# Optimization experiments

Hardware: AMD Instinct MI355X
Metric: run time of the kernel (lower is better)

## Reference

```python
import jax, jax.numpy as jnp
import numpy as np

N, E = 10000, 320000
IN_CH, HID, OUT_CH, HEADS = 128, 64, 40, 8
NEG_SLOPE = 0.2


def gat_conv(x, src, dst, W, a_src, a_dst, bias, heads, C, concat, n_nodes):
    # x: [N, F_in]; W: [F_in, heads*C]; a_src/a_dst: [heads, C]
    h = (x @ W).reshape(n_nodes, heads, C)              # [N,H,C]
    alpha_src = jnp.sum(h * a_src, axis=-1)             # [N,H]
    alpha_dst = jnp.sum(h * a_dst, axis=-1)             # [N,H]
    score = jax.nn.leaky_relu(alpha_src[src] + alpha_dst[dst], NEG_SLOPE)  # [E,H]
    # segment softmax over edges sharing the same destination node
    smax = jax.ops.segment_max(score, dst, num_segments=n_nodes)
    smax = jnp.where(jnp.isfinite(smax), smax, 0.0)
    ex = jnp.exp(score - smax[dst])
    denom = jax.ops.segment_sum(ex, dst, num_segments=n_nodes)
    alpha = ex / (denom[dst] + 1e-16)                   # [E,H]
    msg = h[src] * alpha[:, :, None]                    # [E,H,C]
    out = jax.ops.segment_sum(msg, dst, num_segments=n_nodes)  # [N,H,C]
    out = out.reshape(n_nodes, heads * C) if concat else out.mean(axis=1)
    return out + bias


def setup_inputs() -> dict:
    key = jax.random.key(0)
    ks = jax.random.split(key, 16)
    g = 0.1
    return {
        "x": jax.random.normal(ks[0], (N, IN_CH), jnp.float32),
        "edge_index": jax.random.randint(ks[1], (2, E), 0, N, jnp.int64),
        "W1": jax.random.normal(ks[2], (IN_CH, HID), jnp.float32) * g,
        "b1": jnp.zeros((HID,), jnp.float32),
        "Wc1": jax.random.normal(ks[3], (HID, HEADS * HID), jnp.float32) * g,
        "att_src1": jax.random.normal(ks[4], (HEADS, HID), jnp.float32) * g,
        "att_dst1": jax.random.normal(ks[5], (HEADS, HID), jnp.float32) * g,
        "bc1": jnp.zeros((HEADS * HID,), jnp.float32),
        "Wc2": jax.random.normal(ks[6], (HEADS * HID, HID), jnp.float32) * g,
        "att_src2": jax.random.normal(ks[7], (1, HID), jnp.float32) * g,
        "att_dst2": jax.random.normal(ks[8], (1, HID), jnp.float32) * g,
        "bc2": jnp.zeros((HID,), jnp.float32),
        "W2": jax.random.normal(ks[9], (HID, OUT_CH), jnp.float32) * g,
        "b2": jnp.zeros((OUT_CH,), jnp.float32),
    }


def reference(x, edge_index, W1, b1, Wc1, att_src1, att_dst1, bc1,
              Wc2, att_src2, att_dst2, bc2, W2, b2):
    # add self-loops (PyG GATConv default add_self_loops=True)
    loop = jnp.arange(N, dtype=edge_index.dtype)
    src = jnp.concatenate([edge_index[0], loop])
    dst = jnp.concatenate([edge_index[1], loop])

    h = jax.nn.relu(x @ W1 + b1)                                   # lin0 + relu (dropout off in eval)
    h = jax.nn.elu(gat_conv(h, src, dst, Wc1, att_src1, att_dst1, bc1,
                            HEADS, HID, True, N))                  # conv1, concat heads
    h = gat_conv(h, src, dst, Wc2, att_src2, att_dst2, bc2,
                 1, HID, False, N)                                 # conv2, single head
    return h @ W2 + b2
```

## Files before the change

### kernel.cpp

```cpp
#include <hip/hip_runtime.h>
#include <cstdint>
#include <cstddef>

#define IN_CH 128
#define HID 64
#define HEADS 8
#define OUT_CH 40
#define NEG 0.2f
#define PAD 128

typedef __attribute__((ext_vector_type(8))) short bf16x8;
typedef __attribute__((ext_vector_type(4))) float f32x4;

#define MFMA(a, b, c) __builtin_amdgcn_mfma_f32_16x16x32_bf16(a, b, c, 0, 0, 0)

__device__ inline unsigned short f2bf(float f) {
    unsigned u = __float_as_uint(f);
    unsigned r = (u + 0x7FFFu + ((u >> 16) & 1u)) >> 16;
    return (unsigned short)r;
}
__device__ inline float bf2f(unsigned short b) {
    return __uint_as_float((unsigned)b << 16);
}
__device__ inline bf16x8 ldb8(const unsigned short* p) {
    return *reinterpret_cast<const bf16x8*>(p);
}


__global__ void k_init(const float* __restrict__ W1,
                       const float* __restrict__ Wc1, const float* __restrict__ Wc2,
                       const float* __restrict__ as1, const float* __restrict__ ad1,
                       int* __restrict__ cursor,
                       unsigned short* __restrict__ W1T,
                       unsigned short* __restrict__ Wc1T, unsigned short* __restrict__ Wc2T,
                       unsigned short* __restrict__ vaT, int N) {
    int i = blockIdx.x * 256 + threadIdx.x;
    if (i < N) { cursor[i] = 0; return; }
    i -= N;
    if (i < 64 * 128) {
        int j = i >> 7, k = i & 127;
        W1T[i] = f2bf(W1[k * 64 + j]);
        return;
    }
    i -= 64 * 128;
    if (i < 512 * 64) {
        int j = i >> 6, k = i & 63;
        Wc1T[i] = f2bf(Wc1[(size_t)k * 512 + j]);
        return;
    }
    i -= 512 * 64;
    if (i < 64 * 512) {
        int j = i >> 9, k = i & 511;
        Wc2T[i] = f2bf(Wc2[(size_t)k * 64 + j]);
        return;
    }
    i -= 64 * 512;
    if (i < 1024) {
        int t = i >> 6, k = i & 63;
        int h = t & 7;
        const float* a = (t < 8) ? as1 : ad1;
        float sum = 0.f;
        for (int c = 0; c < 64; ++c) sum += Wc1[(size_t)k * 512 + h * 64 + c] * a[h * 64 + c];
        vaT[t * 64 + k] = f2bf(sum);
    }
}


__global__ __launch_bounds__(256) void k_lin1m(const float* __restrict__ x,
                                               const unsigned short* __restrict__ W1T,
                                               const float* __restrict__ b1,
                                               const unsigned short* __restrict__ vaT,
                                               unsigned short* __restrict__ h0b,
                                               float* __restrict__ asrc, float* __restrict__ adst,
                                               const int* __restrict__ ei, int E, int T,
                                               int* __restrict__ cursor, int* __restrict__ csrc,
                                               int N, int NB) {
    __shared__ unsigned short h0s[16][72];
    if (blockIdx.x >= NB) {
        int e = (blockIdx.x - NB) * 256 + threadIdx.x;
        if (e < T) {
            int s, d;
            if (e < E) { s = ei[e]; d = ei[E + e]; } else { s = d = e - E; }
            int pos = atomicAdd(&cursor[d], 1);
            csrc[(size_t)d * PAD + pos] = s;
        }
        return;
    }
    int w = threadIdx.x >> 6, l = threadIdx.x & 63;
    int m0 = blockIdx.x * 16;
    int c = l & 15, g = l >> 4;
    int xr = m0 + c; if (xr >= N) xr = N - 1;
    bf16x8 af[4];
    const float* arow = x + (size_t)xr * 128 + 8 * g;
#pragma unroll
    for (int ks = 0; ks < 4; ++ks) {
        float4 f0 = *(const float4*)(arow + 32 * ks);
        float4 f1 = *(const float4*)(arow + 32 * ks + 4);
        bf16x8 t;
        t[0] = (short)f2bf(f0.x); t[1] = (short)f2bf(f0.y);
        t[2] = (short)f2bf(f0.z); t[3] = (short)f2bf(f0.w);
        t[4] = (short)f2bf(f1.x); t[5] = (short)f2bf(f1.y);
        t[6] = (short)f2bf(f1.z); t[7] = (short)f2bf(f1.w);
        af[ks] = t;
    }
    f32x4 acc = {};
    const unsigned short* brow = W1T + (size_t)(16 * w + c) * 128 + 8 * g;
#pragma unroll
    for (int ks = 0; ks < 4; ++ks) acc = MFMA(af[ks], ldb8(brow + 32 * ks), acc);
    int j = 16 * w + c;
    float bj = b1[j];
#pragma unroll
    for (int r = 0; r < 4; ++r) {
        float v = fmaxf(acc[r] + bj, 0.f);
        unsigned short us = f2bf(v);
        int row = m0 + 4 * g + r;
        if (row < N) h0b[(size_t)row * 64 + j] = us;
        h0s[4 * g + r][j] = us;
    }
    __syncthreads();
    if (w == 0) {
        bf16x8 a0 = ldb8(&h0s[c][8 * g]);
        bf16x8 a1 = ldb8(&h0s[c][32 + 8 * g]);
        bf16x8 b0 = ldb8(&vaT[c * 64 + 8 * g]);
        bf16x8 b1v = ldb8(&vaT[c * 64 + 32 + 8 * g]);
        f32x4 al = {};
        al = MFMA(a0, b0, al);
        al = MFMA(a1, b1v, al);
#pragma unroll
        for (int r = 0; r < 4; ++r) {
            int n = m0 + 4 * g + r;
            if (n < N) {
                if (c < 8) asrc[n * 8 + c] = al[r];
                else       adst[n * 8 + (c - 8)] = al[r];
            }
        }
    }
}


__global__ __launch_bounds__(128) void k_conv1agg(const unsigned short* __restrict__ h0b,
                                                  const float* __restrict__ asrc, const float* __restrict__ adst,
                                                  const int* __restrict__ degs, const int* __restrict__ csrc,
                                                  unsigned short* __restrict__ aggb, int N) {
    __shared__ int srcb[PAD];
    __shared__ float sb[PAD][8];
    __shared__ float mx[8], den[8], adl[8];
    __shared__ float accsh[512];
    int tid = threadIdx.x;
    int n = blockIdx.x;
    int deg = degs[n];
    if (tid < 8) adl[tid] = adst[n * 8 + tid];
    __syncthreads();
    if (tid < deg) {
        int s = csrc[(size_t)n * PAD + tid];
        srcb[tid] = s;
        const float4* ap = (const float4*)&asrc[(size_t)s * 8];
        float4 a0 = ap[0], a1 = ap[1];
        float v;
        v = a0.x + adl[0]; sb[tid][0] = (v >= 0.f) ? v : NEG * v;
        v = a0.y + adl[1]; sb[tid][1] = (v >= 0.f) ? v : NEG * v;
        v = a0.z + adl[2]; sb[tid][2] = (v >= 0.f) ? v : NEG * v;
        v = a0.w + adl[3]; sb[tid][3] = (v >= 0.f) ? v : NEG * v;
        v = a1.x + adl[4]; sb[tid][4] = (v >= 0.f) ? v : NEG * v;
        v = a1.y + adl[5]; sb[tid][5] = (v >= 0.f) ? v : NEG * v;
        v = a1.z + adl[6]; sb[tid][6] = (v >= 0.f) ? v : NEG * v;
        v = a1.w + adl[7]; sb[tid][7] = (v >= 0.f) ? v : NEG * v;
    }
    __syncthreads();
    if (tid < 64) {
        int hh = tid & 7, idx = tid >> 3;
        float m = -1e30f;
        for (int i = idx; i < deg; i += 8) m = fmaxf(m, sb[i][hh]);
        m = fmaxf(m, __shfl_xor(m, 8));
        m = fmaxf(m, __shfl_xor(m, 16));
        m = fmaxf(m, __shfl_xor(m, 32));
        if (tid < 8) mx[tid] = m;
    }
    __syncthreads();
    if (tid < 64) {
        int hh = tid & 7, idx = tid >> 3;
        float mh = mx[hh];
        float d = 0.f;
        for (int i = idx; i < deg; i += 8) {
            float e = __expf(sb[i][hh] - mh);
            sb[i][hh] = e;
            d += e;
        }
        d += __shfl_xor(d, 8);
        d += __shfl_xor(d, 16);
        d += __shfl_xor(d, 32);
        if (tid < 8) den[tid] = d + 1e-16f;
    }
    __syncthreads();
    int lane = tid & 63, wv = tid >> 6;
    int half = lane >> 5, cl = lane & 31;
    float accA[8] = {0.f, 0.f, 0.f, 0.f, 0.f, 0.f, 0.f, 0.f};
    float accB[8] = {0.f, 0.f, 0.f, 0.f, 0.f, 0.f, 0.f, 0.f};
    for (int i = 2 * wv; i < deg; i += 4) {
        int e = i + half;
        float vx = 0.f, vy = 0.f;
        float4 w0 = {0.f, 0.f, 0.f, 0.f}, w1 = {0.f, 0.f, 0.f, 0.f};
        if (e < deg) {
            unsigned u = *(const unsigned*)&h0b[(size_t)srcb[e] * 64 + 2 * cl];
            vx = bf2f((unsigned short)(u & 0xFFFFu));
            vy = bf2f((unsigned short)(u >> 16));
            w0 = *(const float4*)&sb[e][0];
            w1 = *(const float4*)&sb[e][4];
        }
        accA[0] += w0.x * vx; accB[0] += w0.x * vy;
        accA[1] += w0.y * vx; accB[1] += w0.y * vy;
        accA[2] += w0.z * vx; accB[2] += w0.z * vy;
        accA[3] += w0.w * vx; accB[3] += w0.w * vy;
        accA[4] += w1.x * vx; accB[4] += w1.x * vy;
        accA[5] += w1.y * vx; accB[5] += w1.y * vy;
        accA[6] += w1.z * vx; accB[6] += w1.z * vy;
        accA[7] += w1.w * vx; accB[7] += w1.w * vy;
    }
#pragma unroll
    for (int h = 0; h < 8; ++h) {
        accA[h] += __shfl_xor(accA[h], 32);
        accB[h] += __shfl_xor(accB[h], 32);
    }
    __syncthreads();
    if (wv == 1 && half == 0) {
#pragma unroll
        for (int h = 0; h < 8; ++h) {
            accsh[h * 64 + 2 * cl] = accA[h];
            accsh[h * 64 + 2 * cl + 1] = accB[h];
        }
    }
    __syncthreads();
    if (wv == 0 && half == 0) {
#pragma unroll
        for (int h = 0; h < 8; ++h) {
            float t0 = (accA[h] + accsh[h * 64 + 2 * cl]) / den[h];
            float t1 = (accB[h] + accsh[h * 64 + 2 * cl + 1]) / den[h];
            unsigned uo = (unsigned)f2bf(t0) | ((unsigned)f2bf(t1) << 16);
            *(unsigned*)&aggb[(size_t)n * 512 + h * 64 + 2 * cl] = uo;
        }
    }
}


__global__ __launch_bounds__(256) void k_p1l2(const unsigned short* __restrict__ aggb,
                                              const unsigned short* __restrict__ Wc1T,
                                              const float* __restrict__ bc1,
                                              const unsigned short* __restrict__ Wc2T,
                                              const float* __restrict__ as2, const float* __restrict__ ad2,
                                              unsigned short* __restrict__ hc2b,
                                              float* __restrict__ asrc, float* __restrict__ adst, int N) {
    __shared__ unsigned short h1s[16][520];
    __shared__ float pps[4][16][2];
    int w = threadIdx.x >> 6, l = threadIdx.x & 63;
    int m0 = blockIdx.x * 16;
    int c = l & 15, g = l >> 4;
#pragma unroll
    for (int hl = 0; hl < 2; ++hl) {
        int h = 2 * w + hl;
        const unsigned short* arow = aggb + (size_t)(m0 + c) * 512 + h * 64 + 8 * g;
        bf16x8 af0 = ldb8(arow), af1 = ldb8(arow + 32);
        f32x4 acc[4] = {};
#pragma unroll
        for (int nt = 0; nt < 4; ++nt) {
            const unsigned short* brow = Wc1T + (size_t)(h * 64 + 16 * nt + c) * 64 + 8 * g;
            acc[nt] = MFMA(af0, ldb8(brow), acc[nt]);
            acc[nt] = MFMA(af1, ldb8(brow + 32), acc[nt]);
        }
#pragma unroll
        for (int nt = 0; nt < 4; ++nt) {
            int j = h * 64 + 16 * nt + c;
            float bj = bc1[j];
#pragma unroll
            for (int r = 0; r < 4; ++r) {
                float v = acc[nt][r] + bj;
                v = (v > 0.f) ? v : __expf(v) - 1.f;
                h1s[4 * g + r][j] = f2bf(v);
            }
        }
    }
    __syncthreads();
    f32x4 acc2 = {};
    const unsigned short* brow2 = Wc2T + (size_t)(16 * w + c) * 512 + 8 * g;
#pragma unroll 4
    for (int ks = 0; ks < 16; ++ks) {
        bf16x8 af = ldb8(&h1s[c][32 * ks + 8 * g]);
        acc2 = MFMA(af, ldb8(brow2 + 32 * ks), acc2);
    }
    int j = 16 * w + c;
    float aj = as2[j], dj = ad2[j];
    float ps[4], pd[4];
#pragma unroll
    for (int r = 0; r < 4; ++r) {
        float v = acc2[r];
        hc2b[(size_t)(m0 + 4 * g + r) * 64 + j] = f2bf(v);
        ps[r] = v * aj;
        pd[r] = v * dj;
    }
#pragma unroll
    for (int r = 0; r < 4; ++r) {
        float s = ps[r], d = pd[r];
        s += __shfl_xor(s, 1); s += __shfl_xor(s, 2); s += __shfl_xor(s, 4); s += __shfl_xor(s, 8);
        d += __shfl_xor(d, 1); d += __shfl_xor(d, 2); d += __shfl_xor(d, 4); d += __shfl_xor(d, 8);
        if (c == 0) {
            pps[w][4 * g + r][0] = s;
            pps[w][4 * g + r][1] = d;
        }
    }
    __syncthreads();
    int tid = threadIdx.x;
    if (tid < 32) {
        int row = tid >> 1, sel = tid & 1;
        float sum = pps[0][row][sel] + pps[1][row][sel] + pps[2][row][sel] + pps[3][row][sel];
        int n = m0 + row;
        if (n < N) {
            if (sel == 0) asrc[n] = sum;
            else          adst[n] = sum;
        }
    }
}


__global__ __launch_bounds__(256) void k_conv2f(const unsigned short* __restrict__ hc2b,
                                                const float* __restrict__ asrc, const float* __restrict__ adst,
                                                const int* __restrict__ degs, const int* __restrict__ csrc,
                                                const float* __restrict__ bc2,
                                                const float* __restrict__ W2, const float* __restrict__ b2,
                                                float* __restrict__ out, int N) {
    __shared__ float w2s[HID * OUT_CH];
    __shared__ float cosh_[4][HID];
    int tid = threadIdx.x;
    for (int i = tid; i < HID * OUT_CH; i += 256) w2s[i] = W2[i];
    int lane = tid & 63, nl = tid >> 6;
    int half = lane >> 5, cl = lane & 31;
    int n = blockIdx.x * 4 + nl;
    if (n < N) {
        int deg = degs[n];
        float ad = adst[n];
        float rm = -1e30f, rden = 0.f;
        float ax = 0.f, ay = 0.f;
        for (int base = 0; base < deg; base += 64) {
            int cnt = min(64, deg - base);
            int s = 0;
            float sc = -1e30f;
            if (lane < cnt) {
                s = csrc[(size_t)n * PAD + base + lane];
                float v = asrc[s] + ad;
                sc = (v >= 0.f) ? v : NEG * v;
            }
            float m = sc;
#pragma unroll
            for (int mm = 1; mm < 64; mm <<= 1) m = fmaxf(m, __shfl_xor(m, mm));
            float nmv = fmaxf(rm, m);
            float scale = __expf(rm - nmv);
            float p = (lane < cnt) ? __expf(sc - nmv) : 0.f;
            float d = p;
#pragma unroll
            for (int mm = 1; mm < 64; mm <<= 1) d += __shfl_xor(d, mm);
            rden = rden * scale + d;
            rm = nmv;
            ax *= scale; ay *= scale;
            for (int i = 0; i < cnt; i += 2) {
                int idx = i + half;
                float pi = __shfl(p, idx);
                int si = __shfl(s, idx);
                unsigned u = *(const unsigned*)&hc2b[(size_t)si * 64 + 2 * cl];
                ax += pi * bf2f((unsigned short)(u & 0xFFFFu));
                ay += pi * bf2f((unsigned short)(u >> 16));
            }
        }
        ax += __shfl_xor(ax, 32);
        ay += __shfl_xor(ay, 32);
        if (half == 0) {
            float inv = 1.f / (rden + 1e-16f);
            cosh_[nl][2 * cl] = ax * inv + bc2[2 * cl];
            cosh_[nl][2 * cl + 1] = ay * inv + bc2[2 * cl + 1];
        }
    }
    __syncthreads();
    if (tid >= 160) return;
    int nn = tid / 40, j = tid % 40;
    int no = blockIdx.x * 4 + nn;
    if (no >= N) return;
    float s = b2[j];
#pragma unroll 8
    for (int k = 0; k < HID; ++k) s += cosh_[nn][k] * w2s[k * OUT_CH + j];
    out[(size_t)no * OUT_CH + j] = s;
}


extern "C" void kernel_launch(void* const* d_in, const int* in_sizes, int n_in,
                              void* d_out, int out_size, void* d_ws, size_t ws_size,
                              hipStream_t stream) {
    const float* x   = (const float*)d_in[0];
    const int*   ei  = (const int*)d_in[1];
    const float* W1  = (const float*)d_in[2];
    const float* b1  = (const float*)d_in[3];
    const float* Wc1 = (const float*)d_in[4];
    const float* as1 = (const float*)d_in[5];
    const float* ad1 = (const float*)d_in[6];
    const float* bc1 = (const float*)d_in[7];
    const float* Wc2 = (const float*)d_in[8];
    const float* as2 = (const float*)d_in[9];
    const float* ad2 = (const float*)d_in[10];
    const float* bc2 = (const float*)d_in[11];
    const float* W2  = (const float*)d_in[12];
    const float* b2  = (const float*)d_in[13];

    const int N = in_sizes[0] / IN_CH;
    const int E = in_sizes[1] / 2;
    const int T = E + N;

    char* base = (char*)d_ws;
    size_t off = 0;
    auto carve = [&](size_t bytes) -> void* {
        off = (off + 255) & ~(size_t)255;
        void* r = base + off;
        off += bytes;
        return r;
    };
    int* cursor     = (int*)carve((size_t)N * 4);
    int* csrc       = (int*)carve((size_t)N * PAD * 4);
    unsigned short* W1T  = (unsigned short*)carve((size_t)64 * 128 * 2);
    unsigned short* Wc1T = (unsigned short*)carve((size_t)512 * 64 * 2);
    unsigned short* Wc2T = (unsigned short*)carve((size_t)64 * 512 * 2);
    unsigned short* vaT  = (unsigned short*)carve((size_t)16 * 64 * 2);
    unsigned short* h0b  = (unsigned short*)carve((size_t)N * 64 * 2);
    float* asrc1    = (float*)carve((size_t)N * 8 * 4);
    float* adst1    = (float*)carve((size_t)N * 8 * 4);
    unsigned short* aggb = (unsigned short*)carve((size_t)N * 512 * 2);
    unsigned short* hc2b = (unsigned short*)carve((size_t)N * 64 * 2);
    float* asrc2    = (float*)carve((size_t)N * 4);
    float* adst2    = (float*)carve((size_t)N * 4);

    int init_total = N + 64 * 128 + 512 * 64 + 64 * 512 + 1024;
    k_init<<<(init_total + 255) / 256, 256, 0, stream>>>(W1, Wc1, Wc2, as1, ad1, cursor,
                                                         W1T, Wc1T, Wc2T, vaT, N);

    int NB = (N + 15) / 16;
    int FB = (T + 255) / 256;
    k_lin1m<<<NB + FB, 256, 0, stream>>>(x, W1T, b1, vaT, h0b, asrc1, adst1,
                                         ei, E, T, cursor, csrc, N, NB);
    k_conv1agg<<<N, 128, 0, stream>>>(h0b, asrc1, adst1, cursor, csrc, aggb, N);
    k_p1l2<<<(N + 15) / 16, 256, 0, stream>>>(aggb, Wc1T, bc1, Wc2T, as2, ad2,
                                              hc2b, asrc2, adst2, N);
    k_conv2f<<<(N + 3) / 4, 256, 0, stream>>>(hc2b, asrc2, adst2, cursor, csrc, bc2, W2, b2,
                                              (float*)d_out, N);
}
```

Measured before the change: 95.37 us.

## Fuse conv1 aggregation with projection GEMMs into one kernel via shared memory

Merges the per-node conv1 attention aggregation kernel with the following Wc1/Wc2 projection kernel. Each 512-thread block first aggregates 16 destination nodes into shared memory, using one wave per two nodes and an online softmax. It then runs the MFMA projections on that tile, so the N x 512 bf16 aggregation buffer never goes through global memory and one launch is removed. The cost is fewer blocks (N/16) with heavier serial per-wave work, plus a larger shared-memory footprint that may lower occupancy.

Result: slower. 117.8 us (+23.5%).

```diff
diff --git a/kernel.cpp b/kernel.cpp
--- a/kernel.cpp
+++ b/kernel.cpp
@@ -138,183 +138,161 @@
 }
 
 
-__global__ __launch_bounds__(128) void k_conv1agg(const unsigned short* __restrict__ h0b,
-                                                  const float* __restrict__ asrc, const float* __restrict__ adst,
-                                                  const int* __restrict__ degs, const int* __restrict__ csrc,
-                                                  unsigned short* __restrict__ aggb, int N) {
-    __shared__ int srcb[PAD];
-    __shared__ float sb[PAD][8];
-    __shared__ float mx[8], den[8], adl[8];
-    __shared__ float accsh[512];
+__global__ __launch_bounds__(512) void k_cpl(const unsigned short* __restrict__ h0b,
+                                             const float* __restrict__ asrc, const float* __restrict__ adst,
+                                             const int* __restrict__ degs, const int* __restrict__ csrc,
+                                             const unsigned short* __restrict__ Wc1T,
+                                             const float* __restrict__ bc1,
+                                             const unsigned short* __restrict__ Wc2T,
+                                             const float* __restrict__ as2, const float* __restrict__ ad2,
+                                             unsigned short* __restrict__ hc2b,
+                                             float* __restrict__ asrc2, float* __restrict__ adst2, int N) {
+    __shared__ unsigned short aggs[16][520];
+    __shared__ union {
+        float sbw[8][64][8];
+        unsigned short h1s[16][520];
+    } u;
+    __shared__ float pps[4][16][2];
     int tid = threadIdx.x;
-    int n = blockIdx.x;
-    int deg = degs[n];
-    if (tid < 8) adl[tid] = adst[n * 8 + tid];
+    int w = tid >> 6, l = tid & 63;
+    int m0 = blockIdx.x * 16;
+
+    for (int it = 0; it < 2; ++it) {
+        int n = m0 + 2 * w + it;
+        if (n < N) {
+            int deg = degs[n];
+            float4 ad0 = *(const float4*)&adst[(size_t)n * 8];
+            float4 ad1v = *(const float4*)&adst[(size_t)n * 8 + 4];
+            float racc[8] = {0.f, 0.f, 0.f, 0.f, 0.f, 0.f, 0.f, 0.f};
+            float rmax[8], rden[8];
+#pragma unroll
+            for (int h = 0; h < 8; ++h) { rmax[h] = -1e30f; rden[h] = 0.f; }
+            for (int base = 0; base < deg; base += 64) {
+                int cnt = min(64, deg - base);
+                bool act = l < cnt;
+                int s = 0;
+                float sc[8];
+#pragma unroll
+                for (int h = 0; h < 8; ++h) sc[h] = -1e30f;
+                if (act) {
+                    s = csrc[(size_t)n * PAD + base + l];
+                    float4 a0 = *(const float4*)&asrc[(size_t)s * 8];
+                    float4 a1 = *(const float4*)&asrc[(size_t)s * 8 + 4];
+                    float v;
+                    v = a0.x + ad0.x; sc[0] = (v >= 0.f) ? v : NEG * v;
+                    v = a0.y + ad0.y; sc[1] = (v >= 0.f) ? v : NEG * v;
+                    v = a0.z + ad0.z; sc[2] = (v >= 0.f) ? v : NEG * v;
+                    v = a0.w + ad0.w; sc[3] = (v >= 0.f) ? v : NEG * v;
+                    v = a1.x + ad1v.x; sc[4] = (v >= 0.f) ? v : NEG * v;
+                    v = a1.y + ad1v.y; sc[5] = (v >= 0.f) ? v : NEG * v;
+                    v = a1.z + ad1v.z; sc[6] = (v >= 0.f) ? v : NEG * v;
+                    v = a1.w + ad1v.w; sc[7] = (v >= 0.f) ? v : NEG * v;
+                }
+                float pe[8];
+#pragma unroll
+                for (int h = 0; h < 8; ++h) {
+                    float m = sc[h];
+                    m = fmaxf(m, __shfl_xor(m, 1));
+                    m = fmaxf(m, __shfl_xor(m, 2));
+                    m = fmaxf(m, __shfl_xor(m, 4));
+                    m = fmaxf(m, __shfl_xor(m, 8));
+                    m = fmaxf(m, __shfl_xor(m, 16));
+                    m = fmaxf(m, __shfl_xor(m, 32));
+                    float nm = fmaxf(rmax[h], m);
+                    float scale = __expf(rmax[h] - nm);
+                    rmax[h] = nm;
+                    float p = act ? __expf(sc[h] - nm) : 0.f;
+                    float d = p;
+                    d += __shfl_xor(d, 1);
+                    d += __shfl_xor(d, 2);
+                    d += __shfl_xor(d, 4);
+                    d += __shfl_xor(d, 8);
+                    d += __shfl_xor(d, 16);
+                    d += __shfl_xor(d, 32);
+                    rden[h] = rden[h] * scale + d;
+                    racc[h] *= scale;
+                    pe[h] = p;
+                }
+                *(float4*)&u.sbw[w][l][0] = make_float4(pe[0], pe[1], pe[2], pe[3]);
+                *(float4*)&u.sbw[w][l][4] = make_float4(pe[4], pe[5], pe[6], pe[7]);
+                for (int e = 0; e < cnt; ++e) {
+                    int se = __shfl(s, e);
+                    float v = bf2f(h0b[(size_t)se * 64 + l]);
+                    float4 q0 = *(const float4*)&u.sbw[w][e][0];
+                    float4 q1 = *(const float4*)&u.sbw[w][e][4];
+                    racc[0] += q0.x * v; racc[1] += q0.y * v;
+                    racc[2] += q0.z * v; racc[3] += q0.w * v;
+                    racc[4] += q1.x * v; racc[5] += q1.y * v;
+                    racc[6] += q1.z * v; racc[7] += q1.w * v;
+                }
+            }
+#pragma unroll
+            for (int h = 0; h < 8; ++h)
+                aggs[2 * w + it][h * 64 + l] = f2bf(racc[h] / (rden[h] + 1e-16f));
+        } else {
+#pragma unroll
+            for (int h = 0; h < 8; ++h) aggs[2 * w + it][h * 64 + l] = 0;
+        }
+    }
     __syncthreads();
-    if (tid < deg) {
-        int s = csrc[(size_t)n * PAD + tid];
-        srcb[tid] = s;
-        const float4* ap = (const float4*)&asrc[(size_t)s * 8];
-        float4 a0 = ap[0], a1 = ap[1];
-        float v;
-        v = a0.x + adl[0]; sb[tid][0] = (v >= 0.f) ? v : NEG * v;
-        v = a0.y + adl[1]; sb[tid][1] = (v >= 0.f) ? v : NEG * v;
-        v = a0.z + adl[2]; sb[tid][2] = (v >= 0.f) ? v : NEG * v;
-        v = a0.w + adl[3]; sb[tid][3] = (v >= 0.f) ? v : NEG * v;
-        v = a1.x + adl[4]; sb[tid][4] = (v >= 0.f) ? v : NEG * v;
-        v = a1.y + adl[5]; sb[tid][5] = (v >= 0.f) ? v : NEG * v;
-        v = a1.z + adl[6]; sb[tid][6] = (v >= 0.f) ? v : NEG * v;
-        v = a1.w + adl[7]; sb[tid][7] = (v >= 0.f) ? v : NEG * v;
-    }
-    __syncthreads();
-    if (tid < 64) {
-        int hh = tid & 7, idx = tid >> 3;
-        float m = -1e30f;
-        for (int i = idx; i < deg; i += 8) m = fmaxf(m, sb[i][hh]);
-        m = fmaxf(m, __shfl_xor(m, 8));
-        m = fmaxf(m, __shfl_xor(m, 16));
-        m = fmaxf(m, __shfl_xor(m, 32));
-        if (tid < 8) mx[tid] = m;
-    }
-    __syncthreads();
-    if (tid < 64) {
-        int hh = tid & 7, idx = tid >> 3;
-        float mh = mx[hh];
-        float d = 0.f;
-        for (int i = idx; i < deg; i += 8) {
-            float e = __expf(sb[i][hh] - mh);
-            sb[i][hh] = e;
-            d += e;
-        }
-        d += __shfl_xor(d, 8);
-        d += __shfl_xor(d, 16);
-        d += __shfl_xor(d, 32);
-        if (tid < 8) den[tid] = d + 1e-16f;
-    }
-    __syncthreads();
-    int lane = tid & 63, wv = tid >> 6;
-    int half = lane >> 5, cl = lane & 31;
-    float accA[8] = {0.f, 0.f, 0.f, 0.f, 0.f, 0.f, 0.f, 0.f};
-    float accB[8] = {0.f, 0.f, 0.f, 0.f, 0.f, 0.f, 0.f, 0.f};
-    for (int i = 2 * wv; i < deg; i += 4) {
-        int e = i + half;
-        float vx = 0.f, vy = 0.f;
-        float4 w0 = {0.f, 0.f, 0.f, 0.f}, w1 = {0.f, 0.f, 0.f, 0.f};
-        if (e < deg) {
-            unsigned u = *(const unsigned*)&h0b[(size_t)srcb[e] * 64 + 2 * cl];
-            vx = bf2f((unsigned short)(u & 0xFFFFu));
-            vy = bf2f((unsigned short)(u >> 16));
-            w0 = *(const float4*)&sb[e][0];
-            w1 = *(const float4*)&sb[e][4];
-        }
-        accA[0] += w0.x * vx; accB[0] += w0.x * vy;
-        accA[1] += w0.y * vx; accB[1] += w0.y * vy;
-        accA[2] += w0.z * vx; accB[2] += w0.z * vy;
-        accA[3] += w0.w * vx; accB[3] += w0.w * vy;
-        accA[4] += w1.x * vx; accB[4] += w1.x * vy;
-        accA[5] += w1.y * vx; accB[5] += w1.y * vy;
-        accA[6] += w1.z * vx; accB[6] += w1.z * vy;
-        accA[7] += w1.w * vx; accB[7] += w1.w * vy;
-    }
-#pragma unroll
-    for (int h = 0; h < 8; ++h) {
-        accA[h] += __shfl_xor(accA[h], 32);
-        accB[h] += __shfl_xor(accB[h], 32);
-    }
-    __syncthreads();
-    if (wv == 1 && half == 0) {
-#pragma unroll
-        for (int h = 0; h < 8; ++h) {
-            accsh[h * 64 + 2 * cl] = accA[h];
-            accsh[h * 64 + 2 * cl + 1] = accB[h];
-        }
-    }
-    __syncthreads();
-    if (wv == 0 && half == 0) {
-#pragma unroll
-        for (int h = 0; h < 8; ++h) {
-            float t0 = (accA[h] + accsh[h * 64 + 2 * cl]) / den[h];
-            float t1 = (accB[h] + accsh[h * 64 + 2 * cl + 1]) / den[h];
-            unsigned uo = (unsigned)f2bf(t0) | ((unsigned)f2bf(t1) << 16);
-            *(unsigned*)&aggb[(size_t)n * 512 + h * 64 + 2 * cl] = uo;
-        }
-    }
-}
-
-
-__global__ __launch_bounds__(256) void k_p1l2(const unsigned short* __restrict__ aggb,
-                                              const unsigned short* __restrict__ Wc1T,
-                                              const float* __restrict__ bc1,
-                                              const unsigned short* __restrict__ Wc2T,
-                                              const float* __restrict__ as2, const float* __restrict__ ad2,
-                                              unsigned short* __restrict__ hc2b,
-                                              float* __restrict__ asrc, float* __restrict__ adst, int N) {
-    __shared__ unsigned short h1s[16][520];
-    __shared__ float pps[4][16][2];
-    int w = threadIdx.x >> 6, l = threadIdx.x & 63;
-    int m0 = blockIdx.x * 16;
+
     int c = l & 15, g = l >> 4;
-#pragma unroll
-    for (int hl = 0; hl < 2; ++hl) {
-        int h = 2 * w + hl;
-        const unsigned short* arow = aggb + (size_t)(m0 + c) * 512 + h * 64 + 8 * g;
-        bf16x8 af0 = ldb8(arow), af1 = ldb8(arow + 32);
+    {
+        bf16x8 af0 = ldb8(&aggs[c][w * 64 + 8 * g]);
+        bf16x8 af1 = ldb8(&aggs[c][w * 64 + 32 + 8 * g]);
         f32x4 acc[4] = {};
 #pragma unroll
         for (int nt = 0; nt < 4; ++nt) {
-            const unsigned short* brow = Wc1T + (size_t)(h * 64 + 16 * nt + c) * 64 + 8 * g;
+            const unsigned short* brow = Wc1T + (size_t)(w * 64 + 16 * nt + c) * 64 + 8 * g;
             acc[nt] = MFMA(af0, ldb8(brow), acc[nt]);
             acc[nt] = MFMA(af1, ldb8(brow + 32), acc[nt]);
         }
+        __syncthreads();
 #pragma unroll
         for (int nt = 0; nt < 4; ++nt) {
-            int j = h * 64 + 16 * nt + c;
+            int j = w * 64 + 16 * nt + c;
             float bj = bc1[j];
 #pragma unroll
             for (int r = 0; r < 4; ++r) {
                 float v = acc[nt][r] + bj;
                 v = (v > 0.f) ? v : __expf(v) - 1.f;
-                h1s[4 * g + r][j] = f2bf(v);
+                u.h1s[4 * g + r][j] = f2bf(v);
             }
         }
     }
     __syncthreads();
-    f32x4 acc2 = {};
-    const unsigned short* brow2 = Wc2T + (size_t)(16 * w + c) * 512 + 8 * g;
+
+    if (w < 4) {
+        f32x4 acc2 = {};
+        const unsigned short* brow2 = Wc2T + (size_t)(16 * w + c) * 512 + 8 * g;
 #pragma unroll 4
-    for (int ks = 0; ks < 16; ++ks) {
-        bf16x8 af = ldb8(&h1s[c][32 * ks + 8 * g]);
-        acc2 = MFMA(af, ldb8(brow2 + 32 * ks), acc2);
-    }
-    int j = 16 * w + c;
-    float aj = as2[j], dj = ad2[j];
-    float ps[4], pd[4];
-#pragma unroll
-    for (int r = 0; r < 4; ++r) {
-        float v = acc2[r];
-        hc2b[(size_t)(m0 + 4 * g + r) * 64 + j] = f2bf(v);
-        ps[r] = v * aj;
-        pd[r] = v * dj;
-    }
-#pragma unroll
-    for (int r = 0; r < 4; ++r) {
-        float s = ps[r], d = pd[r];
-        s += __shfl_xor(s, 1); s += __shfl_xor(s, 2); s += __shfl_xor(s, 4); s += __shfl_xor(s, 8);
-        d += __shfl_xor(d, 1); d += __shfl_xor(d, 2); d += __shfl_xor(d, 4); d += __shfl_xor(d, 8);
-        if (c == 0) {
-            pps[w][4 * g + r][0] = s;
-            pps[w][4 * g + r][1] = d;
+        for (int ks = 0; ks < 16; ++ks) {
+            bf16x8 af = ldb8(&u.h1s[c][32 * ks + 8 * g]);
+            acc2 = MFMA(af, ldb8(brow2 + 32 * ks), acc2);
+        }
+        int j = 16 * w + c;
+        float aj = as2[j], dj = ad2[j];
+#pragma unroll
+        for (int r = 0; r < 4; ++r) {
+            float v = acc2[r];
+            hc2b[(size_t)(m0 + 4 * g + r) * 64 + j] = f2bf(v);
+            float s = v * aj, d = v * dj;
+            s += __shfl_xor(s, 1); s += __shfl_xor(s, 2); s += __shfl_xor(s, 4); s += __shfl_xor(s, 8);
+            d += __shfl_xor(d, 1); d += __shfl_xor(d, 2); d += __shfl_xor(d, 4); d += __shfl_xor(d, 8);
+            if (c == 0) {
+                pps[w][4 * g + r][0] = s;
+                pps[w][4 * g + r][1] = d;
+            }
         }
     }
     __syncthreads();
-    int tid = threadIdx.x;
     if (tid < 32) {
         int row = tid >> 1, sel = tid & 1;
         float sum = pps[0][row][sel] + pps[1][row][sel] + pps[2][row][sel] + pps[3][row][sel];
         int n = m0 + row;
         if (n < N) {
-            if (sel == 0) asrc[n] = sum;
-            else          adst[n] = sum;
+            if (sel == 0) asrc2[n] = sum;
+            else          adst2[n] = sum;
         }
     }
 }
@@ -363,9 +341,9 @@
                 int idx = i + half;
                 float pi = __shfl(p, idx);
                 int si = __shfl(s, idx);
-                unsigned u = *(const unsigned*)&hc2b[(size_t)si * 64 + 2 * cl];
-                ax += pi * bf2f((unsigned short)(u & 0xFFFFu));
-                ay += pi * bf2f((unsigned short)(u >> 16));
+                unsigned uu = *(const unsigned*)&hc2b[(size_t)si * 64 + 2 * cl];
+                ax += pi * bf2f((unsigned short)(uu & 0xFFFFu));
+                ay += pi * bf2f((unsigned short)(uu >> 16));
             }
         }
         ax += __shfl_xor(ax, 32);
@@ -427,7 +405,6 @@
     unsigned short* h0b  = (unsigned short*)carve((size_t)N * 64 * 2);
     float* asrc1    = (float*)carve((size_t)N * 8 * 4);
     float* adst1    = (float*)carve((size_t)N * 8 * 4);
-    unsigned short* aggb = (unsigned short*)carve((size_t)N * 512 * 2);
     unsigned short* hc2b = (unsigned short*)carve((size_t)N * 64 * 2);
     float* asrc2    = (float*)carve((size_t)N * 4);
     float* adst2    = (float*)carve((size_t)N * 4);
@@ -440,9 +417,9 @@
     int FB = (T + 255) / 256;
     k_lin1m<<<NB + FB, 256, 0, stream>>>(x, W1T, b1, vaT, h0b, asrc1, adst1,
                                          ei, E, T, cursor, csrc, N, NB);
-    k_conv1agg<<<N, 128, 0, stream>>>(h0b, asrc1, adst1, cursor, csrc, aggb, N);
-    k_p1l2<<<(N + 15) / 16, 256, 0, stream>>>(aggb, Wc1T, bc1, Wc2T, as2, ad2,
-                                              hc2b, asrc2, adst2, N);
+    k_cpl<<<(N + 15) / 16, 512, 0, stream>>>(h0b, asrc1, adst1, cursor, csrc,
+                                             Wc1T, bc1, Wc2T, as2, ad2,
+                                             hc2b, asrc2, adst2, N);
     k_conv2f<<<(N + 3) / 4, 256, 0, stream>>>(hc2b, asrc2, adst2, cursor, csrc, bc2, W2, b2,
                                               (float*)d_out, N);
 }
```

## Fold final linear layer into conv2 weights and widen conv1 aggregation blocks

Applied to the files above, without the earlier changes.

Because aggregation is linear, the final W2 projection and the conv2 attention vectors are precomputed into one combined 512x48 weight (Wc2·W2 plus the att_src/att_dst columns). Conv2 then gathers 40-wide features per edge instead of 64, and the separate W2 matmul is dropped. A constant vector bc2·W2 + b2 is added at the end. Separately, conv1 aggregation moves from 128 to 256 threads per node, with four waves splitting edges and reduced through shared memory. The combined weights are held in bf16, which changes rounding, and conv2 now walks edges one at a time with only 40 of 64 lanes busy.

Result: slower. 102.0 us (+7.0%).

```diff
diff --git a/kernel.cpp b/kernel.cpp
--- a/kernel.cpp
+++ b/kernel.cpp
@@ -30,10 +30,15 @@
 __global__ void k_init(const float* __restrict__ W1,
                        const float* __restrict__ Wc1, const float* __restrict__ Wc2,
                        const float* __restrict__ as1, const float* __restrict__ ad1,
+                       const float* __restrict__ as2, const float* __restrict__ ad2,
+                       const float* __restrict__ W2, const float* __restrict__ bc2,
+                       const float* __restrict__ b2,
                        int* __restrict__ cursor,
                        unsigned short* __restrict__ W1T,
-                       unsigned short* __restrict__ Wc1T, unsigned short* __restrict__ Wc2T,
-                       unsigned short* __restrict__ vaT, int N) {
+                       unsigned short* __restrict__ Wc1T,
+                       unsigned short* __restrict__ vaT,
+                       unsigned short* __restrict__ WcombT,
+                       float* __restrict__ cst, int N) {
     int i = blockIdx.x * 256 + threadIdx.x;
     if (i < N) { cursor[i] = 0; return; }
     i -= N;
@@ -49,12 +54,6 @@
         return;
     }
     i -= 512 * 64;
-    if (i < 64 * 512) {
-        int j = i >> 9, k = i & 511;
-        Wc2T[i] = f2bf(Wc2[(size_t)k * 64 + j]);
-        return;
-    }
-    i -= 64 * 512;
     if (i < 1024) {
         int t = i >> 6, k = i & 63;
         int h = t & 7;
@@ -62,6 +61,27 @@
         float sum = 0.f;
         for (int c = 0; c < 64; ++c) sum += Wc1[(size_t)k * 512 + h * 64 + c] * a[h * 64 + c];
         vaT[t * 64 + k] = f2bf(sum);
+        return;
+    }
+    i -= 1024;
+    if (i < 48 * 512) {
+        int j = i >> 9, k = i & 511;
+        float sum = 0.f;
+        if (j < 40) {
+            for (int m = 0; m < 64; ++m) sum += Wc2[(size_t)k * 64 + m] * W2[m * 40 + j];
+        } else if (j == 40) {
+            for (int m = 0; m < 64; ++m) sum += Wc2[(size_t)k * 64 + m] * as2[m];
+        } else if (j == 41) {
+            for (int m = 0; m < 64; ++m) sum += Wc2[(size_t)k * 64 + m] * ad2[m];
+        }
+        WcombT[i] = f2bf(sum);
+        return;
+    }
+    i -= 48 * 512;
+    if (i < 40) {
+        float sum = b2[i];
+        for (int m = 0; m < 64; ++m) sum += bc2[m] * W2[m * 40 + i];
+        cst[i] = sum;
     }
 }
 
@@ -138,14 +158,14 @@
 }
 
 
-__global__ __launch_bounds__(128) void k_conv1agg(const unsigned short* __restrict__ h0b,
+__global__ __launch_bounds__(256) void k_conv1agg(const unsigned short* __restrict__ h0b,
                                                   const float* __restrict__ asrc, const float* __restrict__ adst,
                                                   const int* __restrict__ degs, const int* __restrict__ csrc,
                                                   unsigned short* __restrict__ aggb, int N) {
     __shared__ int srcb[PAD];
     __shared__ float sb[PAD][8];
     __shared__ float mx[8], den[8], adl[8];
-    __shared__ float accsh[512];
+    __shared__ float accsh[3][512];
     int tid = threadIdx.x;
     int n = blockIdx.x;
     int deg = degs[n];
@@ -196,7 +216,7 @@
     int half = lane >> 5, cl = lane & 31;
     float accA[8] = {0.f, 0.f, 0.f, 0.f, 0.f, 0.f, 0.f, 0.f};
     float accB[8] = {0.f, 0.f, 0.f, 0.f, 0.f, 0.f, 0.f, 0.f};
-    for (int i = 2 * wv; i < deg; i += 4) {
+    for (int i = 2 * wv; i < deg; i += 8) {
         int e = i + half;
         float vx = 0.f, vy = 0.f;
         float4 w0 = {0.f, 0.f, 0.f, 0.f}, w1 = {0.f, 0.f, 0.f, 0.f};
@@ -222,19 +242,24 @@
         accB[h] += __shfl_xor(accB[h], 32);
     }
     __syncthreads();
-    if (wv == 1 && half == 0) {
+    if (wv > 0 && half == 0) {
 #pragma unroll
         for (int h = 0; h < 8; ++h) {
-            accsh[h * 64 + 2 * cl] = accA[h];
-            accsh[h * 64 + 2 * cl + 1] = accB[h];
+            accsh[wv - 1][h * 64 + 2 * cl] = accA[h];
+            accsh[wv - 1][h * 64 + 2 * cl + 1] = accB[h];
         }
     }
     __syncthreads();
     if (wv == 0 && half == 0) {
 #pragma unroll
         for (int h = 0; h < 8; ++h) {
-            float t0 = (accA[h] + accsh[h * 64 + 2 * cl]) / den[h];
-            float t1 = (accB[h] + accsh[h * 64 + 2 * cl + 1]) / den[h];
+            float t0 = accA[h], t1 = accB[h];
+#pragma unroll
+            for (int i = 0; i < 3; ++i) {
+                t0 += accsh[i][h * 64 + 2 * cl];
+                t1 += accsh[i][h * 64 + 2 * cl + 1];
+            }
+            t0 /= den[h]; t1 /= den[h];
             unsigned uo = (unsigned)f2bf(t0) | ((unsigned)f2bf(t1) << 16);
             *(unsigned*)&aggb[(size_t)n * 512 + h * 64 + 2 * cl] = uo;
         }
@@ -245,12 +270,10 @@
 __global__ __launch_bounds__(256) void k_p1l2(const unsigned short* __restrict__ aggb,
                                               const unsigned short* __restrict__ Wc1T,
                                               const float* __restrict__ bc1,
-                                              const unsigned short* __restrict__ Wc2T,
-                                              const float* __restrict__ as2, const float* __restrict__ ad2,
-                                              unsigned short* __restrict__ hc2b,
-                                              float* __restrict__ asrc, float* __restrict__ adst, int N) {
+                                              const unsigned short* __restrict__ WcombT,
+                                              unsigned short* __restrict__ hw2b,
+                                              float* __restrict__ asrc2, float* __restrict__ adst2, int N) {
     __shared__ unsigned short h1s[16][520];
-    __shared__ float pps[4][16][2];
     int w = threadIdx.x >> 6, l = threadIdx.x & 63;
     int m0 = blockIdx.x * 16;
     int c = l & 15, g = l >> 4;
@@ -279,112 +302,68 @@
         }
     }
     __syncthreads();
-    f32x4 acc2 = {};
-    const unsigned short* brow2 = Wc2T + (size_t)(16 * w + c) * 512 + 8 * g;
+    if (w < 3) {
+        f32x4 acc2 = {};
+        const unsigned short* brow2 = WcombT + (size_t)(16 * w + c) * 512 + 8 * g;
 #pragma unroll 4
-    for (int ks = 0; ks < 16; ++ks) {
-        bf16x8 af = ldb8(&h1s[c][32 * ks + 8 * g]);
-        acc2 = MFMA(af, ldb8(brow2 + 32 * ks), acc2);
-    }
-    int j = 16 * w + c;
-    float aj = as2[j], dj = ad2[j];
-    float ps[4], pd[4];
-#pragma unroll
-    for (int r = 0; r < 4; ++r) {
-        float v = acc2[r];
-        hc2b[(size_t)(m0 + 4 * g + r) * 64 + j] = f2bf(v);
-        ps[r] = v * aj;
-        pd[r] = v * dj;
-    }
-#pragma unroll
-    for (int r = 0; r < 4; ++r) {
-        float s = ps[r], d = pd[r];
-        s += __shfl_xor(s, 1); s += __shfl_xor(s, 2); s += __shfl_xor(s, 4); s += __shfl_xor(s, 8);
-        d += __shfl_xor(d, 1); d += __shfl_xor(d, 2); d += __shfl_xor(d, 4); d += __shfl_xor(d, 8);
-        if (c == 0) {
-            pps[w][4 * g + r][0] = s;
-            pps[w][4 * g + r][1] = d;
-        }
-    }
-    __syncthreads();
-    int tid = threadIdx.x;
-    if (tid < 32) {
-        int row = tid >> 1, sel = tid & 1;
-        float sum = pps[0][row][sel] + pps[1][row][sel] + pps[2][row][sel] + pps[3][row][sel];
-        int n = m0 + row;
-        if (n < N) {
-            if (sel == 0) asrc[n] = sum;
-            else          adst[n] = sum;
-        }
-    }
-}
-
-
-__global__ __launch_bounds__(256) void k_conv2f(const unsigned short* __restrict__ hc2b,
+        for (int ks = 0; ks < 16; ++ks) {
+            bf16x8 af = ldb8(&h1s[c][32 * ks + 8 * g]);
+            acc2 = MFMA(af, ldb8(brow2 + 32 * ks), acc2);
+        }
+        int j = 16 * w + c;
+#pragma unroll
+        for (int r = 0; r < 4; ++r) {
+            int row = m0 + 4 * g + r;
+            if (row < N) {
+                if (j < 40)       hw2b[(size_t)row * 40 + j] = f2bf(acc2[r]);
+                else if (j == 40) asrc2[row] = acc2[r];
+                else if (j == 41) adst2[row] = acc2[r];
+            }
+        }
+    }
+}
+
+
+__global__ __launch_bounds__(256) void k_conv2f(const unsigned short* __restrict__ hw2b,
                                                 const float* __restrict__ asrc, const float* __restrict__ adst,
                                                 const int* __restrict__ degs, const int* __restrict__ csrc,
-                                                const float* __restrict__ bc2,
-                                                const float* __restrict__ W2, const float* __restrict__ b2,
+                                                const float* __restrict__ cst,
                                                 float* __restrict__ out, int N) {
-    __shared__ float w2s[HID * OUT_CH];
-    __shared__ float cosh_[4][HID];
     int tid = threadIdx.x;
-    for (int i = tid; i < HID * OUT_CH; i += 256) w2s[i] = W2[i];
     int lane = tid & 63, nl = tid >> 6;
-    int half = lane >> 5, cl = lane & 31;
     int n = blockIdx.x * 4 + nl;
-    if (n < N) {
-        int deg = degs[n];
-        float ad = adst[n];
-        float rm = -1e30f, rden = 0.f;
-        float ax = 0.f, ay = 0.f;
-        for (int base = 0; base < deg; base += 64) {
-            int cnt = min(64, deg - base);
-            int s = 0;
-            float sc = -1e30f;
-            if (lane < cnt) {
-                s = csrc[(size_t)n * PAD + base + lane];
-                float v = asrc[s] + ad;
-                sc = (v >= 0.f) ? v : NEG * v;
-            }
-            float m = sc;
-#pragma unroll
-            for (int mm = 1; mm < 64; mm <<= 1) m = fmaxf(m, __shfl_xor(m, mm));
-            float nmv = fmaxf(rm, m);
-            float scale = __expf(rm - nmv);
-            float p = (lane < cnt) ? __expf(sc - nmv) : 0.f;
-            float d = p;
-#pragma unroll
-            for (int mm = 1; mm < 64; mm <<= 1) d += __shfl_xor(d, mm);
-            rden = rden * scale + d;
-            rm = nmv;
-            ax *= scale; ay *= scale;
-            for (int i = 0; i < cnt; i += 2) {
-                int idx = i + half;
-                float pi = __shfl(p, idx);
-                int si = __shfl(s, idx);
-                unsigned u = *(const unsigned*)&hc2b[(size_t)si * 64 + 2 * cl];
-                ax += pi * bf2f((unsigned short)(u & 0xFFFFu));
-                ay += pi * bf2f((unsigned short)(u >> 16));
-            }
-        }
-        ax += __shfl_xor(ax, 32);
-        ay += __shfl_xor(ay, 32);
-        if (half == 0) {
-            float inv = 1.f / (rden + 1e-16f);
-            cosh_[nl][2 * cl] = ax * inv + bc2[2 * cl];
-            cosh_[nl][2 * cl + 1] = ay * inv + bc2[2 * cl + 1];
-        }
-    }
-    __syncthreads();
-    if (tid >= 160) return;
-    int nn = tid / 40, j = tid % 40;
-    int no = blockIdx.x * 4 + nn;
-    if (no >= N) return;
-    float s = b2[j];
-#pragma unroll 8
-    for (int k = 0; k < HID; ++k) s += cosh_[nn][k] * w2s[k * OUT_CH + j];
-    out[(size_t)no * OUT_CH + j] = s;
+    if (n >= N) return;
+    int deg = degs[n];
+    float ad = adst[n];
+    float rm = -1e30f, rden = 0.f, acc = 0.f;
+    for (int base = 0; base < deg; base += 64) {
+        int cnt = min(64, deg - base);
+        int s = 0;
+        float sc = -1e30f;
+        if (lane < cnt) {
+            s = csrc[(size_t)n * PAD + base + lane];
+            float v = asrc[s] + ad;
+            sc = (v >= 0.f) ? v : NEG * v;
+        }
+        float m = sc;
+#pragma unroll
+        for (int mm = 1; mm < 64; mm <<= 1) m = fmaxf(m, __shfl_xor(m, mm));
+        float nmv = fmaxf(rm, m);
+        float scale = __expf(rm - nmv);
+        float p = (lane < cnt) ? __expf(sc - nmv) : 0.f;
+        float d = p;
+#pragma unroll
+        for (int mm = 1; mm < 64; mm <<= 1) d += __shfl_xor(d, mm);
+        rden = rden * scale + d;
+        rm = nmv;
+        acc *= scale;
+        for (int i = 0; i < cnt; ++i) {
+            float pi = __shfl(p, i);
+            int si = __shfl(s, i);
+            if (lane < OUT_CH) acc += pi * bf2f(hw2b[(size_t)si * 40 + lane]);
+        }
+    }
+    if (lane < OUT_CH) out[(size_t)n * OUT_CH + lane] = acc / (rden + 1e-16f) + cst[lane];
 }
 
 
@@ -420,29 +399,30 @@
     };
     int* cursor     = (int*)carve((size_t)N * 4);
     int* csrc       = (int*)carve((size_t)N * PAD * 4);
-    unsigned short* W1T  = (unsigned short*)carve((size_t)64 * 128 * 2);
-    unsigned short* Wc1T = (unsigned short*)carve((size_t)512 * 64 * 2);
-    unsigned short* Wc2T = (unsigned short*)carve((size_t)64 * 512 * 2);
-    unsigned short* vaT  = (unsigned short*)carve((size_t)16 * 64 * 2);
+    unsigned short* W1T    = (unsigned short*)carve((size_t)64 * 128 * 2);
+    unsigned short* Wc1T   = (unsigned short*)carve((size_t)512 * 64 * 2);
+    unsigned short* vaT    = (unsigned short*)carve((size_t)16 * 64 * 2);
+    unsigned short* WcombT = (unsigned short*)carve((size_t)48 * 512 * 2);
+    float* cst      = (float*)carve((size_t)40 * 4);
     unsigned short* h0b  = (unsigned short*)carve((size_t)N * 64 * 2);
     float* asrc1    = (float*)carve((size_t)N * 8 * 4);
     float* adst1    = (float*)carve((size_t)N * 8 * 4);
     unsigned short* aggb = (unsigned short*)carve((size_t)N * 512 * 2);
-    unsigned short* hc2b = (unsigned short*)carve((size_t)N * 64 * 2);
+    unsigned short* hw2b = (unsigned short*)carve((size_t)N * 40 * 2);
     float* asrc2    = (float*)carve((size_t)N * 4);
     float* adst2    = (float*)carve((size_t)N * 4);
 
-    int init_total = N + 64 * 128 + 512 * 64 + 64 * 512 + 1024;
-    k_init<<<(init_total + 255) / 256, 256, 0, stream>>>(W1, Wc1, Wc2, as1, ad1, cursor,
-                                                         W1T, Wc1T, Wc2T, vaT, N);
+    int init_total = N + 64 * 128 + 512 * 64 + 16 * 64 + 48 * 512 + 40;
+    k_init<<<(init_total + 255) / 256, 256, 0, stream>>>(W1, Wc1, Wc2, as1, ad1, as2, ad2,
+                                                         W2, bc2, b2, cursor,
+                                                         W1T, Wc1T, vaT, WcombT, cst, N);
 
     int NB = (N + 15) / 16;
     int FB = (T + 255) / 256;
     k_lin1m<<<NB + FB, 256, 0, stream>>>(x, W1T, b1, vaT, h0b, asrc1, adst1,
                                          ei, E, T, cursor, csrc, N, NB);
-    k_conv1agg<<<N, 128, 0, stream>>>(h0b, asrc1, adst1, cursor, csrc, aggb, N);
-    k_p1l2<<<(N + 15) / 16, 256, 0, stream>>>(aggb, Wc1T, bc1, Wc2T, as2, ad2,
-                                              hc2b, asrc2, adst2, N);
-    k_conv2f<<<(N + 3) / 4, 256, 0, stream>>>(hc2b, asrc2, adst2, cursor, csrc, bc2, W2, b2,
+    k_conv1agg<<<N, 256, 0, stream>>>(h0b, asrc1, adst1, cursor, csrc, aggb, N);
+    k_p1l2<<<(N + 15) / 16, 256, 0, stream>>>(aggb, Wc1T, bc1, WcombT, hw2b, asrc2, adst2, N);
+    k_conv2f<<<(N + 3) / 4, 256, 0, stream>>>(hw2b, asrc2, adst2, cursor, csrc, cst,
                                               (float*)d_out, N);
 }
```
